# Optimization experiments

Hardware: AMD Instinct MI355X
Metric: run time of the kernel (lower is better)

The kernel has to match this reference:

```python
import jax, jax.numpy as jnp
import numpy as np

EPS = 1e-5
NUM_PIXELS = 2  # M_Relax window half-width


def _conv(x, w, b, groups=1, pad=0):
    y = jax.lax.conv_general_dilated(
        x, w, (1, 1), [(pad, pad), (pad, pad)],
        dimension_numbers=("NCHW", "OIHW", "NCHW"),
        feature_group_count=groups)
    return y + b[None, :, None, None]


def _bn(x, g, bta, m, v):
    # eval-mode BatchNorm2d with running stats
    inv = jax.lax.rsqrt(v + EPS)
    return g[None, :, None, None] * (x - m[None, :, None, None]) * inv[None, :, None, None] + bta[None, :, None, None]


def _resb(x, w1, b1, w2, b2):
    y = _conv(x, w1, b1, groups=4, pad=1)
    y = jnp.where(y > 0, y, 0.1 * y)  # LeakyReLU(0.1)
    y = _conv(y, w2, b2, groups=4, pad=1)
    return y + x


def _relax(M):
    # M: (N, w, w); sum of shifts +-NUM_PIXELS along the row (dim 1)
    w = M.shape[1]
    P = jnp.pad(M, ((0, 0), (NUM_PIXELS, NUM_PIXELS), (0, 0)))
    out = P[:, 0:w, :]
    for k in range(1, 2 * NUM_PIXELS + 1):
        out = out + P[:, k:k + w, :]
    return out


def setup_inputs() -> dict:
    key = jax.random.key(0)
    ks = jax.random.split(key, 16)
    b, c, h, w = 4, 64, 128, 256
    c2 = 2 * c
    s = 0.05
    inp = {
        "x_left": jax.random.normal(ks[0], (b, c, h, w), jnp.float32),
        "x_right": jax.random.normal(ks[1], (b, c, h, w), jnp.float32),
        "conv1_w": jax.random.normal(ks[2], (c, c, 1, 1), jnp.float32) * s,
        "conv1_b": jnp.zeros((c,), jnp.float32),
        "conv2_w": jax.random.normal(ks[3], (c, c, 1, 1), jnp.float32) * s,
        "conv2_b": jnp.zeros((c,), jnp.float32),
        "bn_g": jnp.ones((c2,), jnp.float32),
        "bn_b": jnp.zeros((c2,), jnp.float32),
        "bn_m": jax.random.normal(ks[4], (c2,), jnp.float32) * 0.1,
        "bn_v": jax.random.uniform(ks[5], (c2,), jnp.float32) + 0.5,
        "rb_w1": jax.random.normal(ks[6], (c2, c2 // 4, 3, 3), jnp.float32) * s,
        "rb_b1": jnp.zeros((c2,), jnp.float32),
        "rb_w2": jax.random.normal(ks[7], (c2, c2 // 4, 3, 3), jnp.float32) * s,
        "rb_b2": jnp.zeros((c2,), jnp.float32),
        "bq_w": jax.random.normal(ks[8], (c, c, 1, 1), jnp.float32) * s,
        "bq_b": jnp.zeros((c,), jnp.float32),
        "bs_w": jax.random.normal(ks[9], (c, c, 1, 1), jnp.float32) * s,
        "bs_b": jnp.zeros((c,), jnp.float32),
    }
    return inp


def reference(x_left, x_right, conv1_w, conv1_b, conv2_w, conv2_b,
              bn_g, bn_b, bn_m, bn_v, rb_w1, rb_b1, rb_w2, rb_b2,
              bq_w, bq_b, bs_w, bs_b):
    b, c, h, w = x_left.shape
    cat_l = jnp.concatenate([_conv(x_left, conv1_w, conv1_b), x_left], axis=1)
    cat_r = jnp.concatenate([_conv(x_right, conv2_w, conv2_b), x_right], axis=1)
    Q = _conv(_resb(_bn(cat_l, bn_g, bn_b, bn_m, bn_v), rb_w1, rb_b1, rb_w2, rb_b2), bq_w, bq_b, groups=2)
    K = _conv(_resb(_bn(cat_r, bn_g, bn_b, bn_m, bn_v), rb_w1, rb_b1, rb_w2, rb_b2), bs_w, bs_b, groups=2)
    Q = Q - Q.mean(axis=3, keepdims=True)
    K = K - K.mean(axis=3, keepdims=True)
    # score: (b*h, w, w) -- per-epipolar-row cross-view attention
    Qr = Q.transpose(0, 2, 3, 1).reshape(b * h, w, c)
    Kr = K.transpose(0, 2, 1, 3).reshape(b * h, c, w)
    score = jnp.matmul(Qr, Kr)
    M_r2l = jax.nn.softmax(score, axis=-1)
    M_l2r = jax.nn.softmax(score.transpose(0, 2, 1), axis=-1)
    # validity maps via relaxed cycle-consistency (detached in original)
    V_l = jnp.einsum("nij,nji->ni", _relax(M_r2l), M_l2r)
    V_r = jnp.einsum("nij,nji->ni", _relax(M_l2r), M_r2l)
    V_l = jax.lax.stop_gradient(V_l).reshape(b, 1, h, w)
    V_r = jax.lax.stop_gradient(V_r).reshape(b, 1, h, w)
    V_l_t = jnp.tanh(5.0 * V_l)
    V_r_t = jnp.tanh(5.0 * V_r)
    xl = x_left.transpose(0, 2, 3, 1).reshape(b * h, w, c)
    xr = x_right.transpose(0, 2, 3, 1).reshape(b * h, w, c)
    x_lT = jnp.matmul(M_r2l, xr).reshape(b, h, w, c).transpose(0, 3, 1, 2)
    x_rT = jnp.matmul(M_l2r, xl).reshape(b, h, w, c).transpose(0, 3, 1, 2)
    out_left = x_left * (1.0 - V_l_t) + x_lT * V_l_t
    out_right = x_right * (1.0 - V_r_t) + x_rT * V_r_t
    return out_left, out_right
```

## Files before the change

kernel.cpp:

```cpp
#include <hip/hip_runtime.h>
#include <math.h>

#define BB 4
#define CC 64
#define C2 128
#define HH 128
#define WW 256
#define NN (BB*HH)
#define EPSBN 1e-5f

typedef _Float16 f16;
typedef _Float16 half8 __attribute__((ext_vector_type(8)));
typedef float f32x4 __attribute__((ext_vector_type(4)));

__global__ __launch_bounds__(256) void k_wprep(
    const float* __restrict__ w1, const float* __restrict__ w2,
    f16* __restrict__ wp1, f16* __restrict__ wp2)
{
    int g = blockIdx.x; int which = blockIdx.y;
    const float* src = which ? w2 : w1;
    f16* dst = which ? wp2 : wp1;
    for (int p = threadIdx.x; p < 9216; p += 256) {
        int mo = p / 288; int kr = p - mo*288;
        int ks = kr >> 5; int ic = kr & 31;
        dst[g*9216 + p] = (f16)src[((g*32 + mo)*32 + ic)*9 + ks];
    }
}

__global__ __launch_bounds__(256) void k_catbn_m(
    const float* __restrict__ x, const float* __restrict__ cw, const float* __restrict__ cb,
    const float* __restrict__ g, const float* __restrict__ bb_, const float* __restrict__ m,
    const float* __restrict__ v, f16* __restrict__ u)
{
    __shared__ f16 Xl[256][72];
    __shared__ f16 Wl[64][72];
    __shared__ float sS[64], sT[64], sS2[64], sT2[64];
    int n = blockIdx.x; int b = n >> 7; int h = n & 127; int t = threadIdx.x;
    for (int p = t; p < 2048; p += 256) {
        int idx = p * 2; int o = idx >> 6, i = idx & 63;
        union { f16 h[2]; unsigned int u1; } pr;
        pr.h[0] = (f16)cw[idx]; pr.h[1] = (f16)cw[idx + 1];
        *(unsigned int*)&Wl[o][i] = pr.u1;
    }
    if (t < 64) {
        float inv = rsqrtf(v[t] + EPSBN); float s = g[t] * inv;
        sS[t] = s; sT[t] = bb_[t] + s * (cb[t] - m[t]);
        float inv2 = rsqrtf(v[t + 64] + EPSBN); float s2 = g[t + 64] * inv2;
        sS2[t] = s2; sT2[t] = bb_[t + 64] - s2 * m[t + 64];
    }
    __syncthreads();
    f16* up = u + ((size_t)(n*256 + t)) * 128;
    for (int c8 = 0; c8 < 8; ++c8) {
        float xv8[8];
#pragma unroll
        for (int j = 0; j < 8; ++j)
            xv8[j] = x[(((b*64 + c8*8 + j)*128 + h) << 8) + t];
        union { f16 h[8]; uint4 v4; } pk;
#pragma unroll
        for (int j = 0; j < 8; ++j) {
            int c = c8*8 + j;
            pk.h[j] = (f16)(sS2[c]*xv8[j] + sT2[c]);
        }
        *(uint4*)(up + 64 + c8*8) = pk.v4;
#pragma unroll
        for (int j2 = 0; j2 < 4; ++j2) {
            union { f16 h[2]; unsigned int u1; } q;
            q.h[0] = (f16)xv8[j2*2]; q.h[1] = (f16)xv8[j2*2 + 1];
            *(unsigned int*)&Xl[t][c8*8 + j2*2] = q.u1;
        }
    }
    __syncthreads();
    int lane = t & 63, wv = t >> 6;
    int m16 = lane & 15, quad = lane >> 4;
    half8 af[4][2], bf[4][2];
#pragma unroll
    for (int mt = 0; mt < 4; ++mt)
#pragma unroll
        for (int kk = 0; kk < 2; ++kk)
            af[mt][kk] = *(const half8*)&Wl[mt*16 + m16][kk*32 + quad*8];
#pragma unroll
    for (int nt = 0; nt < 4; ++nt)
#pragma unroll
        for (int kk = 0; kk < 2; ++kk)
            bf[nt][kk] = *(const half8*)&Xl[wv*64 + nt*16 + m16][kk*32 + quad*8];
    f32x4 acc[4][4] = {};
#pragma unroll
    for (int mt = 0; mt < 4; ++mt)
#pragma unroll
        for (int nt = 0; nt < 4; ++nt) {
            acc[mt][nt] = __builtin_amdgcn_mfma_f32_16x16x32_f16(af[mt][0], bf[nt][0], acc[mt][nt], 0, 0, 0);
            acc[mt][nt] = __builtin_amdgcn_mfma_f32_16x16x32_f16(af[mt][1], bf[nt][1], acc[mt][nt], 0, 0, 0);
        }
#pragma unroll
    for (int mt = 0; mt < 4; ++mt) {
        int ocb = mt*16 + quad*4;
        float s4[4], t4[4];
        *(float4*)s4 = *(const float4*)&sS[ocb];
        *(float4*)t4 = *(const float4*)&sT[ocb];
#pragma unroll
        for (int nt = 0; nt < 4; ++nt) {
            int px = wv*64 + nt*16 + m16;
            union { f16 h[4]; uint2 u2; } ov;
#pragma unroll
            for (int r = 0; r < 4; ++r)
                ov.h[r] = (f16)(s4[r]*acc[mt][nt][r] + t4[r]);
            *(uint2*)(u + ((size_t)(n*256 + px))*128 + ocb) = ov.u2;
        }
    }
}

template<bool LEAKY, bool RES>
__global__ __launch_bounds__(256, 3) void k_conv3r(
    const f16* __restrict__ in, const f16* __restrict__ wp,
    const float* __restrict__ bias, const f16* __restrict__ res,
    f16* __restrict__ out)
{
    __shared__ f16 Xl[4*130*40];
    int b = blockIdx.x >> 6; int h0 = (blockIdx.x & 63) * 2;
    int g = blockIdx.y; int w0 = blockIdx.z * 128;
    int t = threadIdx.x;
    int lane = t & 63, wv = t >> 6;
    int m16 = lane & 15, quad = lane >> 4;
    const f16* wg = wp + g*9216;
    half8 af[2][9];
#pragma unroll
    for (int mt = 0; mt < 2; ++mt)
#pragma unroll
        for (int ks = 0; ks < 9; ++ks)
            af[mt][ks] = *(const half8*)(wg + (mt*16 + m16)*288 + ks*32 + quad*8);
    float bo[2][4];
#pragma unroll
    for (int mt = 0; mt < 2; ++mt)
#pragma unroll
        for (int r = 0; r < 4; ++r)
            bo[mt][r] = bias[g*32 + mt*16 + quad*4 + r];
    for (int idx = t; idx < 2080; idx += 256) {
        int r = idx / 520; int rem = idx - r*520; int p = rem >> 2; int q = rem & 3;
        int hr = h0 + r - 1; int wg2 = w0 + p - 1;
        uint4 val = make_uint4(0,0,0,0);
        if ((unsigned)wg2 < 256u && (unsigned)hr < 128u)
            val = *(const uint4*)(in + ((size_t)((b*128 + hr)*256 + wg2))*128 + g*32 + q*8);
        *(uint4*)&Xl[(r*130 + p)*40 + q*8] = val;
    }
    __syncthreads();
    int px0 = wv*32 + m16;
#pragma unroll
    for (int rr = 0; rr < 2; ++rr) {
        f32x4 acc[2][2] = {};
#pragma unroll
        for (int ks = 0; ks < 9; ++ks) {
            int ky = ks / 3, kx = ks - ky*3;
            half8 bf0 = *(const half8*)&Xl[((rr + ky)*130 + px0 + kx)*40 + quad*8];
            half8 bf1 = *(const half8*)&Xl[((rr + ky)*130 + px0 + 16 + kx)*40 + quad*8];
            acc[0][0] = __builtin_amdgcn_mfma_f32_16x16x32_f16(af[0][ks], bf0, acc[0][0], 0, 0, 0);
            acc[0][1] = __builtin_amdgcn_mfma_f32_16x16x32_f16(af[0][ks], bf1, acc[0][1], 0, 0, 0);
            acc[1][0] = __builtin_amdgcn_mfma_f32_16x16x32_f16(af[1][ks], bf0, acc[1][0], 0, 0, 0);
            acc[1][1] = __builtin_amdgcn_mfma_f32_16x16x32_f16(af[1][ks], bf1, acc[1][1], 0, 0, 0);
        }
        int h = h0 + rr;
#pragma unroll
        for (int mt = 0; mt < 2; ++mt)
#pragma unroll
            for (int nt = 0; nt < 2; ++nt) {
                int px = w0 + wv*32 + nt*16 + m16;
                int oc = g*32 + mt*16 + quad*4;
                size_t off = ((size_t)((b*128 + h)*256 + px))*128 + oc;
                float rv4[4] = {0.f, 0.f, 0.f, 0.f};
                if (RES) {
                    union { f16 h[4]; uint2 v2; } rrd;
                    rrd.v2 = *(const uint2*)(res + off);
#pragma unroll
                    for (int r = 0; r < 4; ++r) rv4[r] = (float)rrd.h[r];
                }
                union { f16 h[4]; uint2 v2; } ov;
#pragma unroll
                for (int r = 0; r < 4; ++r) {
                    float y = acc[mt][nt][r] + bo[mt][r];
                    if (LEAKY) y = y > 0.f ? y : 0.1f*y;
                    if (RES) y += rv4[r];
                    ov.h[r] = (f16)y;
                }
                *(uint2*)(out + off) = ov.v2;
            }
    }
}

__global__ __launch_bounds__(256, 2) void k_conv1x1m(
    const f16* __restrict__ in, const float* __restrict__ wgt,
    f16* __restrict__ outq)
{
    __shared__ f16 Xl[256][72];
    __shared__ f16 Wl[64][72];
    __shared__ float partial[4][64];
    __shared__ float meanS[64];
    int n = blockIdx.x; int t = threadIdx.x;
    int lane = t & 63, wv = t >> 6;
    int m16 = lane & 15, quad = lane >> 4;
    for (int p = t; p < 2048; p += 256) {
        int idx = p * 2; int o = idx >> 6, i = idx & 63;
        union { f16 h[2]; unsigned int u1; } pr;
        pr.h[0] = (f16)wgt[idx]; pr.h[1] = (f16)wgt[idx + 1];
        *(unsigned int*)&Wl[o][i] = pr.u1;
    }
    f32x4 acc[4][4] = {};
    const f16* rp = in + ((size_t)n*256 + t)*128;
    for (int g = 0; g < 2; ++g) {
#pragma unroll
        for (int i8 = 0; i8 < 8; ++i8)
            *(uint4*)&Xl[t][i8*8] = *(const uint4*)(rp + g*64 + i8*8);
        __syncthreads();
        half8 af[2][2], bf[4][2];
#pragma unroll
        for (int ml = 0; ml < 2; ++ml)
#pragma unroll
            for (int kk = 0; kk < 2; ++kk)
                af[ml][kk] = *(const half8*)&Wl[g*32 + ml*16 + m16][kk*32 + quad*8];
#pragma unroll
        for (int nt = 0; nt < 4; ++nt)
#pragma unroll
            for (int kk = 0; kk < 2; ++kk)
                bf[nt][kk] = *(const half8*)&Xl[wv*64 + nt*16 + m16][kk*32 + quad*8];
#pragma unroll
        for (int ml = 0; ml < 2; ++ml)
#pragma unroll
            for (int nt = 0; nt < 4; ++nt) {
                int mt = g*2 + ml;
                acc[mt][nt] = __builtin_amdgcn_mfma_f32_16x16x32_f16(af[ml][0], bf[nt][0], acc[mt][nt], 0, 0, 0);
                acc[mt][nt] = __builtin_amdgcn_mfma_f32_16x16x32_f16(af[ml][1], bf[nt][1], acc[mt][nt], 0, 0, 0);
            }
        __syncthreads();
    }
#pragma unroll
    for (int mt = 0; mt < 4; ++mt)
#pragma unroll
        for (int r = 0; r < 4; ++r) {
            float s = acc[mt][0][r] + acc[mt][1][r] + acc[mt][2][r] + acc[mt][3][r];
            s += __shfl_xor(s, 1); s += __shfl_xor(s, 2);
            s += __shfl_xor(s, 4); s += __shfl_xor(s, 8);
            if (m16 == 0) partial[wv][mt*16 + quad*4 + r] = s;
        }
    __syncthreads();
    if (t < 64)
        meanS[t] = (partial[0][t] + partial[1][t] + partial[2][t] + partial[3][t]) * (1.0f/256.0f);
    __syncthreads();
    f16* qp = outq + ((size_t)n*256)*64;
#pragma unroll
    for (int mt = 0; mt < 4; ++mt) {
        int ocb = mt*16 + quad*4;
        float m4[4]; *(float4*)m4 = *(const float4*)&meanS[ocb];
#pragma unroll
        for (int nt = 0; nt < 4; ++nt) {
            int px = wv*64 + nt*16 + m16;
            union { f16 h[4]; uint2 u2; } ov;
#pragma unroll
            for (int r = 0; r < 4; ++r)
                ov.h[r] = (f16)(acc[mt][nt][r] - m4[r]);
            *(uint2*)(qp + (size_t)px*64 + ocb) = ov.u2;
        }
    }
}

template<int RIGHT>
__device__ __forceinline__ void attn_pass(
    const char* Sl, char* pool,
    const float* __restrict__ myM, const float* __restrict__ myI,
    const float* __restrict__ oM,  const float* __restrict__ oI,
    const float* __restrict__ xB, const float* __restrict__ xP,
    float* __restrict__ outp, int b, int h, int t)
{
    f16 (*Pl)[40] = (f16(*)[40])pool;
    f16 (*Xl)[40] = (f16(*)[40])(pool + 20800);
    float* scr = (float*)(pool + 20800);
    float* Vv  = (float*)(pool + 22848);
    int lane = t & 63, wv = t >> 6;
    int m16 = lane & 15, quad = lane >> 4;
    int W = wv * 32;
    int r = t & 255, hc = t >> 8;
    int cbase = hc * 16;
    float rm = myM[r], ri = myI[r];
    int xc = t >> 3, xj = (t & 7) * 4;
    const float* xg = xB + ((size_t)(b*64 + xc)*128 + h)*256;
    f32x4 acc[2][4] = {};
    float vacc = 0.f;
    const char* sb = Sl + (r << 9);
    int xo = (r & 7) << 4;
    for (int kc = 0; kc < 256; kc += 32) {
        float sraw[16];
        if (!RIGHT) {
            half8 v0 = *(const half8*)(sb + (((kc + cbase)*2)      ^ xo));
            half8 v1 = *(const half8*)(sb + (((kc + cbase)*2 + 16) ^ xo));
#pragma unroll
            for (int e = 0; e < 8; ++e) { sraw[e] = (float)v0[e]; sraw[8+e] = (float)v1[e]; }
        } else {
#pragma unroll
            for (int e = 0; e < 16; ++e) {
                int j = kc + cbase + e;
                sraw[e] = (float)*(const f16*)(Sl + (j << 9) + ((r*2) ^ ((j & 7) << 4)));
            }
        }
        {
            half8 p0, p1;
#pragma unroll
            for (int e = 0; e < 8; ++e) p0[e] = (f16)(__expf(sraw[e]     - rm) * ri);
#pragma unroll
            for (int e = 0; e < 8; ++e) p1[e] = (f16)(__expf(sraw[8 + e] - rm) * ri);
            char* pb = (char*)&Pl[r + 2][cbase];
            *(half8*)pb = p0; *(half8*)(pb + 16) = p1;
        }
        {
            float4 x4 = *(const float4*)(xg + kc + xj);
            union { f16 h[4]; uint2 v2; } px;
            px.h[0] = (f16)x4.x; px.h[1] = (f16)x4.y;
            px.h[2] = (f16)x4.z; px.h[3] = (f16)x4.w;
            *(uint2*)&Xl[xc][xj] = px.v2;
        }
        __syncthreads();
#pragma unroll
        for (int j8 = 0; j8 < 2; ++j8) {
            const char* wb = (const char*)&Pl[r][cbase + j8*8];
            half8 w0 = *(const half8*)(wb);
            half8 w1 = *(const half8*)(wb + 80);
            half8 w2 = *(const half8*)(wb + 160);
            half8 w3 = *(const half8*)(wb + 240);
            half8 w4 = *(const half8*)(wb + 320);
            half8 win = w0 + w1 + w2 + w3 + w4;
#pragma unroll
            for (int e = 0; e < 8; ++e) {
                int j = kc + cbase + j8*8 + e;
                float Bv = __expf(sraw[j8*8 + e] - oM[j]) * oI[j];
                vacc = fmaf((float)win[e], Bv, vacc);
            }
        }
        half8 pa[2], xb_[4];
#pragma unroll
        for (int mt = 0; mt < 2; ++mt)
            pa[mt] = *(const half8*)((const char*)&Pl[W + mt*16 + m16 + 2][0] + quad*16);
#pragma unroll
        for (int nt = 0; nt < 4; ++nt)
            xb_[nt] = *(const half8*)((const char*)&Xl[nt*16 + m16][0] + quad*16);
#pragma unroll
        for (int mt = 0; mt < 2; ++mt)
#pragma unroll
            for (int nt = 0; nt < 4; ++nt)
                acc[mt][nt] = __builtin_amdgcn_mfma_f32_16x16x32_f16(pa[mt], xb_[nt], acc[mt][nt], 0, 0, 0);
        __syncthreads();
    }
    scr[hc*256 + r] = vacc;
    __syncthreads();
    if (t < 256) Vv[t] = scr[t] + scr[256 + t];
    __syncthreads();
#pragma unroll
    for (int mt = 0; mt < 2; ++mt) {
        int i0 = W + mt*16 + quad*4;
        float v4[4];
        *(float4*)v4 = *(const float4*)&Vv[i0];
        float tv[4];
#pragma unroll
        for (int rr = 0; rr < 4; ++rr) tv[rr] = tanhf(5.f*v4[rr]);
#pragma unroll
        for (int nt = 0; nt < 4; ++nt) {
            int c = nt*16 + m16;
            size_t base = (((size_t)(b*64 + c)*128 + h) << 8) + i0;
            float xp4[4]; *(float4*)xp4 = *(const float4*)&xP[base];
            float o4[4];
#pragma unroll
            for (int rr = 0; rr < 4; ++rr)
                o4[rr] = xp4[rr]*(1.f - tv[rr]) + acc[mt][nt][rr]*tv[rr];
            *(float4*)&outp[base] = *(float4*)o4;
        }
    }
}

__global__ __launch_bounds__(512, 1) void k_attn2(
    const f16* __restrict__ Q, const f16* __restrict__ K,
    const float* __restrict__ xl, const float* __restrict__ xr,
    float* __restrict__ outL, float* __restrict__ outR)
{
    __shared__ f16 Sl[65536];
    __shared__ __align__(16) char pool[25920];
    __shared__ float rmS[256], riS[256], cmS[256], ciS[256];
    float* colM = (float*)pool;
    float* colS = (float*)(pool + 8192);
    int n = blockIdx.x; int b = n >> 7; int h = n & 127;
    int t = threadIdx.x;
    int lane = t & 63, wv = t >> 6;
    int m16 = lane & 15, quad = lane >> 4;
    int W = wv * 32;

    const f16* ag = Q + (size_t)n*16384;
    const f16* bg = K + (size_t)n*16384;
    half8 af1[2][2];
#pragma unroll
    for (int mt = 0; mt < 2; ++mt)
#pragma unroll
        for (int kk = 0; kk < 2; ++kk)
            af1[mt][kk] = *(const half8*)(ag + (size_t)(W + mt*16 + m16)*64 + kk*32 + quad*8);
    float rowm[8], rows_[8];
#pragma unroll
    for (int i = 0; i < 8; ++i) { rowm[i] = -1e30f; rows_[i] = 0.f; }
    for (int jc = 0; jc < 256; jc += 64) {
        half8 bf1[4][2];
#pragma unroll
        for (int nt = 0; nt < 4; ++nt)
#pragma unroll
            for (int kk = 0; kk < 2; ++kk)
                bf1[nt][kk] = *(const half8*)(bg + (size_t)(jc + nt*16 + m16)*64 + kk*32 + quad*8);
        f32x4 acc1[2][4] = {};
#pragma unroll
        for (int mt = 0; mt < 2; ++mt)
#pragma unroll
            for (int nt = 0; nt < 4; ++nt) {
                acc1[mt][nt] = __builtin_amdgcn_mfma_f32_16x16x32_f16(af1[mt][0], bf1[nt][0], acc1[mt][nt], 0, 0, 0);
                acc1[mt][nt] = __builtin_amdgcn_mfma_f32_16x16x32_f16(af1[mt][1], bf1[nt][1], acc1[mt][nt], 0, 0, 0);
            }
#pragma unroll
        for (int mt = 0; mt < 2; ++mt)
#pragma unroll
            for (int nt = 0; nt < 4; ++nt)
#pragma unroll
                for (int r = 0; r < 4; ++r) {
                    int row = W + mt*16 + quad*4 + r;
                    int col = jc + nt*16 + m16;
                    f16 hv = (f16)acc1[mt][nt][r];
                    *(f16*)((char*)Sl + (row << 9) + ((col*2) ^ ((row & 7) << 4))) = hv;
                    acc1[mt][nt][r] = (float)hv;
                }
#pragma unroll
        for (int mt = 0; mt < 2; ++mt)
#pragma unroll
            for (int r = 0; r < 4; ++r) {
                float lm = fmaxf(fmaxf(acc1[mt][0][r], acc1[mt][1][r]),
                                 fmaxf(acc1[mt][2][r], acc1[mt][3][r]));
                lm = fmaxf(lm, __shfl_xor(lm, 1));
                lm = fmaxf(lm, __shfl_xor(lm, 2));
                lm = fmaxf(lm, __shfl_xor(lm, 4));
                lm = fmaxf(lm, __shfl_xor(lm, 8));
                float le = __expf(acc1[mt][0][r] - lm) + __expf(acc1[mt][1][r] - lm)
                         + __expf(acc1[mt][2][r] - lm) + __expf(acc1[mt][3][r] - lm);
                le += __shfl_xor(le, 1); le += __shfl_xor(le, 2);
                le += __shfl_xor(le, 4); le += __shfl_xor(le, 8);
                int idx = mt*4 + r;
                float nm = fmaxf(rowm[idx], lm);
                rows_[idx] = rows_[idx]*__expf(rowm[idx] - nm) + le*__expf(lm - nm);
                rowm[idx] = nm;
            }
#pragma unroll
        for (int nt = 0; nt < 4; ++nt) {
            float lm = acc1[0][nt][0];
#pragma unroll
            for (int r = 1; r < 4; ++r) lm = fmaxf(lm, acc1[0][nt][r]);
#pragma unroll
            for (int r = 0; r < 4; ++r) lm = fmaxf(lm, acc1[1][nt][r]);
            lm = fmaxf(lm, __shfl_xor(lm, 16));
            lm = fmaxf(lm, __shfl_xor(lm, 32));
            float le = 0.f;
#pragma unroll
            for (int mt2 = 0; mt2 < 2; ++mt2)
#pragma unroll
                for (int r = 0; r < 4; ++r) le += __expf(acc1[mt2][nt][r] - lm);
            le += __shfl_xor(le, 16); le += __shfl_xor(le, 32);
            if (quad == 0) {
                int col = jc + nt*16 + m16;
                colM[wv*256 + col] = lm;
                colS[wv*256 + col] = le;
            }
        }
    }
    if (m16 == 0) {
#pragma unroll
        for (int mt = 0; mt < 2; ++mt)
#pragma unroll
            for (int r = 0; r < 4; ++r) {
                int row = W + mt*16 + quad*4 + r;
                rmS[row] = rowm[mt*4 + r];
                riS[row] = 1.0f / rows_[mt*4 + r];
            }
    }
    __syncthreads();
    if (t < 256) {
        float m = colM[t], s = colS[t];
#pragma unroll
        for (int w = 1; w < 8; ++w) {
            float m2 = colM[w*256 + t], s2 = colS[w*256 + t];
            float nm = fmaxf(m, m2);
            s = s*__expf(m - nm) + s2*__expf(m2 - nm);
            m = nm;
        }
        cmS[t] = m; ciS[t] = 1.0f / s;
    }
    __syncthreads();
    if (t < 10)       *(uint4*)(pool + t*16)           = make_uint4(0,0,0,0);
    else if (t < 20)  *(uint4*)(pool + 20640 + (t-10)*16) = make_uint4(0,0,0,0);

    attn_pass<0>((const char*)Sl, pool, rmS, riS, cmS, ciS, xr, xl, outL, b, h, t);
    __syncthreads();
    attn_pass<1>((const char*)Sl, pool, cmS, ciS, rmS, riS, xl, xr, outR, b, h, t);
}

extern "C" void kernel_launch(void* const* d_in, const int* in_sizes, int n_in,
                              void* d_out, int out_size, void* d_ws, size_t ws_size,
                              hipStream_t stream)
{
    const float* x_left  = (const float*)d_in[0];
    const float* x_right = (const float*)d_in[1];
    const float* conv1_w = (const float*)d_in[2];
    const float* conv1_b = (const float*)d_in[3];
    const float* conv2_w = (const float*)d_in[4];
    const float* conv2_b = (const float*)d_in[5];
    const float* bn_g    = (const float*)d_in[6];
    const float* bn_b    = (const float*)d_in[7];
    const float* bn_m    = (const float*)d_in[8];
    const float* bn_v    = (const float*)d_in[9];
    const float* rb_w1   = (const float*)d_in[10];
    const float* rb_b1   = (const float*)d_in[11];
    const float* rb_w2   = (const float*)d_in[12];
    const float* rb_b2   = (const float*)d_in[13];
    const float* bq_w    = (const float*)d_in[14];
    const float* bs_w    = (const float*)d_in[16];

    f16* W16 = (f16*)d_ws;
    f16* u  = W16;
    f16* y1 = W16 + 16777216;
    f16* r  = W16 + 33554432;
    f16* Qh = W16 + 67108864;
    f16* Kh = W16 + 75497472;
    f16* Wp1 = W16 + 84934656;
    f16* Wp2 = W16 + 84971520;

    float* out_left  = (float*)d_out;
    float* out_right = (float*)d_out + 8388608;

    k_wprep<<<dim3(4, 2), 256, 0, stream>>>(rb_w1, rb_w2, Wp1, Wp2);

    k_catbn_m<<<NN, 256, 0, stream>>>(x_left, conv1_w, conv1_b, bn_g, bn_b, bn_m, bn_v, u);
    k_conv3r<true,  false><<<dim3(256, 4, 2), 256, 0, stream>>>(u, Wp1, rb_b1, nullptr, y1);
    k_conv3r<false, true ><<<dim3(256, 4, 2), 256, 0, stream>>>(y1, Wp2, rb_b2, u, r);
    k_conv1x1m<<<NN, 256, 0, stream>>>(r, bq_w, Qh);

    k_catbn_m<<<NN, 256, 0, stream>>>(x_right, conv2_w, conv2_b, bn_g, bn_b, bn_m, bn_v, u);
    k_conv3r<true,  false><<<dim3(256, 4, 2), 256, 0, stream>>>(u, Wp1, rb_b1, nullptr, y1);
    k_conv3r<false, true ><<<dim3(256, 4, 2), 256, 0, stream>>>(y1, Wp2, rb_b2, u, r);
    k_conv1x1m<<<NN, 256, 0, stream>>>(r, bs_w, Kh);

    k_attn2<<<NN, 512, 0, stream>>>(Qh, Kh, x_left, x_right, out_left, out_right);
}
```

Baseline: 470.5 us.

## Recompute score tiles with MFMA per pass instead of caching full score matrix in LDS

The attention kernel no longer keeps the 128KB fp16 score matrix in shared memory. Each pass recomputes the 32-column score strip with MFMA from Q/K (swapping operands for the right-view pass) and stages it through the existing P buffer. Launch bounds are raised to allow more blocks per CU now that LDS use is small, aiming to improve occupancy and avoid the strided transposed LDS reads. The cost is extra matmul work and global reloads of K/Q per chunk, plus an extra barrier per chunk.

After: 471.2 us. Within noise of the previous version (+0.2%).

```diff
diff --git a/kernel.cpp b/kernel.cpp
--- a/kernel.cpp
+++ b/kernel.cpp
@@ -260,9 +260,8 @@
     }
 }
 
-template<int RIGHT>
-__device__ __forceinline__ void attn_pass(
-    const char* Sl, char* pool,
+__device__ __forceinline__ void attn_pass3(
+    const f16* __restrict__ Ap, const f16* __restrict__ Bp, char* pool,
     const float* __restrict__ myM, const float* __restrict__ myI,
     const float* __restrict__ oM,  const float* __restrict__ oI,
     const float* __restrict__ xB, const float* __restrict__ xP,
@@ -280,39 +279,61 @@
     float rm = myM[r], ri = myI[r];
     int xc = t >> 3, xj = (t & 7) * 4;
     const float* xg = xB + ((size_t)(b*64 + xc)*128 + h)*256;
+    half8 af[2][2];
+#pragma unroll
+    for (int mt = 0; mt < 2; ++mt)
+#pragma unroll
+        for (int kk = 0; kk < 2; ++kk)
+            af[mt][kk] = *(const half8*)(Ap + (size_t)(W + mt*16 + m16)*64 + kk*32 + quad*8);
     f32x4 acc[2][4] = {};
     float vacc = 0.f;
-    const char* sb = Sl + (r << 9);
-    int xo = (r & 7) << 4;
     for (int kc = 0; kc < 256; kc += 32) {
-        float sraw[16];
-        if (!RIGHT) {
-            half8 v0 = *(const half8*)(sb + (((kc + cbase)*2)      ^ xo));
-            half8 v1 = *(const half8*)(sb + (((kc + cbase)*2 + 16) ^ xo));
-#pragma unroll
-            for (int e = 0; e < 8; ++e) { sraw[e] = (float)v0[e]; sraw[8+e] = (float)v1[e]; }
-        } else {
-#pragma unroll
-            for (int e = 0; e < 16; ++e) {
-                int j = kc + cbase + e;
-                sraw[e] = (float)*(const f16*)(Sl + (j << 9) + ((r*2) ^ ((j & 7) << 4)));
-            }
-        }
-        {
-            half8 p0, p1;
-#pragma unroll
-            for (int e = 0; e < 8; ++e) p0[e] = (f16)(__expf(sraw[e]     - rm) * ri);
-#pragma unroll
-            for (int e = 0; e < 8; ++e) p1[e] = (f16)(__expf(sraw[8 + e] - rm) * ri);
-            char* pb = (char*)&Pl[r + 2][cbase];
-            *(half8*)pb = p0; *(half8*)(pb + 16) = p1;
-        }
+        half8 bf[2][2];
+#pragma unroll
+        for (int nt = 0; nt < 2; ++nt)
+#pragma unroll
+            for (int kk = 0; kk < 2; ++kk)
+                bf[nt][kk] = *(const half8*)(Bp + (size_t)(kc + nt*16 + m16)*64 + kk*32 + quad*8);
+        f32x4 s1[2][2] = {};
+#pragma unroll
+        for (int mt = 0; mt < 2; ++mt)
+#pragma unroll
+            for (int nt = 0; nt < 2; ++nt) {
+                s1[mt][nt] = __builtin_amdgcn_mfma_f32_16x16x32_f16(af[mt][0], bf[nt][0], s1[mt][nt], 0, 0, 0);
+                s1[mt][nt] = __builtin_amdgcn_mfma_f32_16x16x32_f16(af[mt][1], bf[nt][1], s1[mt][nt], 0, 0, 0);
+            }
         {
             float4 x4 = *(const float4*)(xg + kc + xj);
             union { f16 h[4]; uint2 v2; } px;
             px.h[0] = (f16)x4.x; px.h[1] = (f16)x4.y;
             px.h[2] = (f16)x4.z; px.h[3] = (f16)x4.w;
             *(uint2*)&Xl[xc][xj] = px.v2;
+        }
+#pragma unroll
+        for (int mt = 0; mt < 2; ++mt)
+#pragma unroll
+            for (int nt = 0; nt < 2; ++nt)
+#pragma unroll
+                for (int rr = 0; rr < 4; ++rr)
+                    Pl[W + mt*16 + quad*4 + rr + 2][nt*16 + m16] = (f16)s1[mt][nt][rr];
+        __syncthreads();
+        float sraw[16];
+        char* pb = (char*)&Pl[r + 2][cbase];
+        {
+            half8 v0 = *(const half8*)pb;
+            half8 v1 = *(const half8*)(pb + 16);
+            half8 p0, p1;
+#pragma unroll
+            for (int e = 0; e < 8; ++e) {
+                sraw[e] = (float)v0[e];
+                p0[e] = (f16)(__expf(sraw[e] - rm) * ri);
+            }
+#pragma unroll
+            for (int e = 0; e < 8; ++e) {
+                sraw[8 + e] = (float)v1[e];
+                p1[e] = (f16)(__expf(sraw[8 + e] - rm) * ri);
+            }
+            *(half8*)pb = p0; *(half8*)(pb + 16) = p1;
         }
         __syncthreads();
 #pragma unroll
@@ -371,12 +392,11 @@
     }
 }
 
-__global__ __launch_bounds__(512, 1) void k_attn2(
+__global__ __launch_bounds__(512, 4) void k_attn3(
     const f16* __restrict__ Q, const f16* __restrict__ K,
     const float* __restrict__ xl, const float* __restrict__ xr,
     float* __restrict__ outL, float* __restrict__ outR)
 {
-    __shared__ f16 Sl[65536];
     __shared__ __align__(16) char pool[25920];
     __shared__ float rmS[256], riS[256], cmS[256], ciS[256];
     float* colM = (float*)pool;
@@ -418,13 +438,8 @@
 #pragma unroll
             for (int nt = 0; nt < 4; ++nt)
 #pragma unroll
-                for (int r = 0; r < 4; ++r) {
-                    int row = W + mt*16 + quad*4 + r;
-                    int col = jc + nt*16 + m16;
-                    f16 hv = (f16)acc1[mt][nt][r];
-                    *(f16*)((char*)Sl + (row << 9) + ((col*2) ^ ((row & 7) << 4))) = hv;
-                    acc1[mt][nt][r] = (float)hv;
-                }
+                for (int r = 0; r < 4; ++r)
+                    acc1[mt][nt][r] = (float)(f16)acc1[mt][nt][r];
 #pragma unroll
         for (int mt = 0; mt < 2; ++mt)
 #pragma unroll
@@ -489,12 +504,12 @@
         cmS[t] = m; ciS[t] = 1.0f / s;
     }
     __syncthreads();
-    if (t < 10)       *(uint4*)(pool + t*16)           = make_uint4(0,0,0,0);
+    if (t < 10)       *(uint4*)(pool + t*16)              = make_uint4(0,0,0,0);
     else if (t < 20)  *(uint4*)(pool + 20640 + (t-10)*16) = make_uint4(0,0,0,0);
 
-    attn_pass<0>((const char*)Sl, pool, rmS, riS, cmS, ciS, xr, xl, outL, b, h, t);
-    __syncthreads();
-    attn_pass<1>((const char*)Sl, pool, cmS, ciS, rmS, riS, xl, xr, outR, b, h, t);
+    attn_pass3(ag, bg, pool, rmS, riS, cmS, ciS, xr, xl, outL, b, h, t);
+    __syncthreads();
+    attn_pass3(bg, ag, pool, cmS, ciS, rmS, riS, xl, xr, outR, b, h, t);
 }
 
 extern "C" void kernel_launch(void* const* d_in, const int* in_sizes, int n_in,
@@ -542,5 +557,5 @@
     k_conv3r<false, true ><<<dim3(256, 4, 2), 256, 0, stream>>>(y1, Wp2, rb_b2, u, r);
     k_conv1x1m<<<NN, 256, 0, stream>>>(r, bs_w, Kh);
 
-    k_attn2<<<NN, 512, 0, stream>>>(Qh, Kh, x_left, x_right, out_left, out_right);
-}
+    k_attn3<<<NN, 512, 0, stream>>>(Qh, Kh, x_left, x_right, out_left, out_right);
+}
```
